# Optimization experiments

Measured on AMD Instinct MI355X. Metric: run time of the kernel, lower is better.

## Reference

```python
import jax, jax.numpy as jnp
import numpy as np

POWER = 2.0
EPS = jnp.float32(np.finfo(np.float32).eps)


def setup_inputs() -> dict:
    key = jax.random.key(0)
    k1, k2, k3 = jax.random.split(key, 3)
    B, P, S = 2, 131072, 512
    station_coords = jax.random.uniform(k1, (B, S, 2), dtype=jnp.float32)
    station_values = jax.random.normal(k2, (B, S), dtype=jnp.float32)
    grid_points = jax.random.uniform(k3, (B, P, 2), dtype=jnp.float32)
    return {
        "station_coords": station_coords,
        "station_values": station_values,
        "grid_points": grid_points,
    }


def reference(station_coords, station_values, grid_points):
    # grid_points: (B, P, 2); station_coords: (B, S, 2)
    diff = grid_points[:, :, None, :] - station_coords[:, None, :, :]  # (B, P, S, 2)
    distances = jnp.sqrt(jnp.sum(diff * diff, axis=-1))                # (B, P, S)
    distances = jnp.where(distances == 0, EPS, distances)
    weights = 1.0 / distances ** POWER                                  # (B, P, S)
    weights_sum = jnp.sum(weights, axis=-1)                             # (B, P)
    interpolated = jnp.sum(weights * station_values[:, None, :], axis=-1) / weights_sum
    return interpolated  # (B, P)
```

## Files before the change

kernel.cpp:

```cpp
#include <hip/hip_runtime.h>


#define BLOCK 256
#define GPT 8
#define NSPLIT 4
#define S_TOT 512
#define S_SUB (S_TOT / NSPLIT)

__device__ __forceinline__ void quad_op(float gx, float gy, float& ws, float& vs,
                                        const float4& f0, const float4& f1,
                                        const float4& f2) {
    constexpr float EPS  = 1.1920928955078125e-07f;
    constexpr float EPS2 = EPS * EPS;
    const float dxa = gx - f0.x, dya = gy - f0.y;
    const float a = fmaf(dxa, dxa, fmaf(dya, dya, EPS2));
    const float dxb = gx - f0.w, dyb = gy - f1.x;
    const float bq = fmaf(dxb, dxb, fmaf(dyb, dyb, EPS2));
    const float dxc = gx - f1.z, dyc = gy - f1.w;
    const float c = fmaf(dxc, dxc, fmaf(dyc, dyc, EPS2));
    const float dxd = gx - f2.y, dyd = gy - f2.z;
    const float d = fmaf(dxd, dxd, fmaf(dyd, dyd, EPS2));
    const float pab = a * bq, pcd = c * d;
    const float sab = a + bq, scd = c + d;
    const float nab = fmaf(f1.y, a, f0.z * bq);
    const float ncd = fmaf(f2.w, c, f2.x * d);
    const float r = __builtin_amdgcn_rcpf(pab * pcd);
    ws = fmaf(fmaf(sab, pcd, scd * pab), r, ws);
    vs = fmaf(fmaf(nab, pcd, ncd * pab), r, vs);
}

__global__ __launch_bounds__(BLOCK) void idw_main(
    const float* __restrict__ station_coords,
    const float* __restrict__ station_values,
    const float* __restrict__ grid_points,
    float2* __restrict__ partial,
    int P, int S) {

    __shared__ float st[S_SUB * 3];

    const int b = blockIdx.y;
    const int z = blockIdx.z;
    const float2* __restrict__ sc2 =
        (const float2*)station_coords + (size_t)b * S + z * S_SUB;
    const float* __restrict__ svb = station_values + (size_t)b * S + z * S_SUB;

    if (threadIdx.x < S_SUB) {
        const int i = threadIdx.x;
        const float2 c = sc2[i];
        st[3 * i + 0] = c.x;
        st[3 * i + 1] = c.y;
        st[3 * i + 2] = svb[i];
    }
    __syncthreads();

    const int tid = blockIdx.x * BLOCK + threadIdx.x;
    const float4* __restrict__ gp4 = (const float4*)grid_points + (size_t)b * (P / 2);
    const float4 ga = gp4[4 * tid + 0];
    const float4 gb = gp4[4 * tid + 1];
    const float4 gc = gp4[4 * tid + 2];
    const float4 gd = gp4[4 * tid + 3];
    const float gx0 = ga.x, gy0 = ga.y, gx1 = ga.z, gy1 = ga.w;
    const float gx2 = gb.x, gy2 = gb.y, gx3 = gb.z, gy3 = gb.w;
    const float gx4 = gc.x, gy4 = gc.y, gx5 = gc.z, gy5 = gc.w;
    const float gx6 = gd.x, gy6 = gd.y, gx7 = gd.z, gy7 = gd.w;

    float ws0 = 0.0f, vs0 = 0.0f, ws1 = 0.0f, vs1 = 0.0f;
    float ws2 = 0.0f, vs2 = 0.0f, ws3 = 0.0f, vs3 = 0.0f;
    float ws4 = 0.0f, vs4 = 0.0f, ws5 = 0.0f, vs5 = 0.0f;
    float ws6 = 0.0f, vs6 = 0.0f, ws7 = 0.0f, vs7 = 0.0f;

    const float4* __restrict__ st4 = (const float4*)st;

#pragma unroll 2
    for (int k = 0; k < S_SUB / 4; ++k) {
        const float4 f0 = st4[3 * k + 0];
        const float4 f1 = st4[3 * k + 1];
        const float4 f2 = st4[3 * k + 2];
        quad_op(gx0, gy0, ws0, vs0, f0, f1, f2);
        quad_op(gx1, gy1, ws1, vs1, f0, f1, f2);
        quad_op(gx2, gy2, ws2, vs2, f0, f1, f2);
        quad_op(gx3, gy3, ws3, vs3, f0, f1, f2);
        quad_op(gx4, gy4, ws4, vs4, f0, f1, f2);
        quad_op(gx5, gy5, ws5, vs5, f0, f1, f2);
        quad_op(gx6, gy6, ws6, vs6, f0, f1, f2);
        quad_op(gx7, gy7, ws7, vs7, f0, f1, f2);
    }

    float4* __restrict__ pb4 =
        (float4*)(partial + ((size_t)(z * 2 + b)) * P);
    pb4[4 * tid + 0] = make_float4(ws0, vs0, ws1, vs1);
    pb4[4 * tid + 1] = make_float4(ws2, vs2, ws3, vs3);
    pb4[4 * tid + 2] = make_float4(ws4, vs4, ws5, vs5);
    pb4[4 * tid + 3] = make_float4(ws6, vs6, ws7, vs7);
}

__global__ __launch_bounds__(256) void idw_combine(
    const float2* __restrict__ partial, float* __restrict__ out, int P) {
    const int gid = blockIdx.x * 256 + threadIdx.x;
    const int pp0 = gid * 4;
    const int b = pp0 >> 17;
    const int p0 = pp0 & (131072 - 1);

    float wa = 0.f, va = 0.f, wb = 0.f, vb = 0.f, wc = 0.f, vc = 0.f, wd = 0.f, vd = 0.f;
#pragma unroll
    for (int z = 0; z < NSPLIT; ++z) {
        const float4* __restrict__ src =
            (const float4*)(partial + ((size_t)(z * 2 + b)) * P);
        const float4 lo = src[p0 / 2 + 0];
        const float4 hi = src[p0 / 2 + 1];
        wa += lo.x; va += lo.y; wb += lo.z; vb += lo.w;
        wc += hi.x; vc += hi.y; wd += hi.z; vd += hi.w;
    }
    ((float4*)out)[((size_t)b * P + p0) / 4] =
        make_float4(va / wa, vb / wb, vc / wc, vd / wd);
}

__global__ __launch_bounds__(BLOCK) void idw_single(
    const float* __restrict__ station_coords, const float* __restrict__ station_values,
    const float* __restrict__ grid_points, float* __restrict__ out, int P, int S) {
    __shared__ float st[S_TOT * 3];
    const int b = blockIdx.y;
    const float2* __restrict__ sc2 = (const float2*)station_coords + (size_t)b * S;
    const float* __restrict__ svb = station_values + (size_t)b * S;
    for (int i = threadIdx.x; i < S; i += BLOCK) {
        const float2 c = sc2[i];
        st[3 * i + 0] = c.x; st[3 * i + 1] = c.y; st[3 * i + 2] = svb[i];
    }
    __syncthreads();
    const int tid = blockIdx.x * BLOCK + threadIdx.x;
    const float4* __restrict__ gp4 = (const float4*)grid_points + (size_t)b * (P / 2);
    const float4 ga = gp4[2 * tid + 0];
    const float4 gb = gp4[2 * tid + 1];
    float ws0 = 0, vs0 = 0, ws1 = 0, vs1 = 0, ws2 = 0, vs2 = 0, ws3 = 0, vs3 = 0;
    const float4* __restrict__ st4 = (const float4*)st;
#pragma unroll 4
    for (int k = 0; k < S_TOT / 4; ++k) {
        const float4 f0 = st4[3 * k + 0];
        const float4 f1 = st4[3 * k + 1];
        const float4 f2 = st4[3 * k + 2];
        quad_op(ga.x, ga.y, ws0, vs0, f0, f1, f2);
        quad_op(ga.z, ga.w, ws1, vs1, f0, f1, f2);
        quad_op(gb.x, gb.y, ws2, vs2, f0, f1, f2);
        quad_op(gb.z, gb.w, ws3, vs3, f0, f1, f2);
    }
    ((float4*)out)[(size_t)b * (P / 4) + tid] =
        make_float4(vs0 / ws0, vs1 / ws1, vs2 / ws2, vs3 / ws3);
}

extern "C" void kernel_launch(void* const* d_in, const int* in_sizes, int n_in,
                              void* d_out, int out_size, void* d_ws, size_t ws_size,
                              hipStream_t stream) {
    const float* station_coords = (const float*)d_in[0];
    const float* station_values = (const float*)d_in[1];
    const float* grid_points    = (const float*)d_in[2];
    float* out = (float*)d_out;

    const int B = 2;
    const int S = in_sizes[1] / B;
    const int P = out_size / B;

    const size_t need = (size_t)NSPLIT * B * P * sizeof(float2);
    if (ws_size >= need && d_ws != nullptr) {
        float2* partial = (float2*)d_ws;
        dim3 grid(P / (BLOCK * GPT), B, NSPLIT);
        idw_main<<<grid, dim3(BLOCK), 0, stream>>>(
            station_coords, station_values, grid_points, partial, P, S);
        dim3 cgrid((B * P) / (256 * 4));
        idw_combine<<<cgrid, dim3(256), 0, stream>>>(partial, out, P);
    } else {
        dim3 grid(P / (BLOCK * 4), B);
        idw_single<<<grid, dim3(BLOCK), 0, stream>>>(
            station_coords, station_values, grid_points, out, P, S);
    }
}
```

Baseline: 87.08 us.

## Read station data directly from global memory and halve station split

The main kernel drops the shared-memory staging of station coordinates and values and instead loads them as float4s straight from global memory. The loads are wave-uniform, so the compiler may turn them into scalar loads. The station split drops from four to two, which halves the partial buffer traffic and the grid size, and launch bounds now request one block per SM. The risk is fewer blocks for latency hiding and dependence on cache hits for the uniform station loads. The fallback single kernel is only restructured with a lambda.

```diff
diff --git a/kernel.cpp b/kernel.cpp
--- a/kernel.cpp
+++ b/kernel.cpp
@@ -3,55 +3,46 @@
 
 #define BLOCK 256
 #define GPT 8
-#define NSPLIT 4
+#define NSPLIT 2
 #define S_TOT 512
 #define S_SUB (S_TOT / NSPLIT)
 
-__device__ __forceinline__ void quad_op(float gx, float gy, float& ws, float& vs,
-                                        const float4& f0, const float4& f1,
-                                        const float4& f2) {
+__device__ __forceinline__ void quad_sm(float gx, float gy, float& ws, float& vs,
+                                        const float4& c0, const float4& c1,
+                                        const float4& vv) {
     constexpr float EPS  = 1.1920928955078125e-07f;
     constexpr float EPS2 = EPS * EPS;
-    const float dxa = gx - f0.x, dya = gy - f0.y;
+    const float dxa = c0.x - gx, dya = c0.y - gy;
     const float a = fmaf(dxa, dxa, fmaf(dya, dya, EPS2));
-    const float dxb = gx - f0.w, dyb = gy - f1.x;
+    const float dxb = c0.z - gx, dyb = c0.w - gy;
     const float bq = fmaf(dxb, dxb, fmaf(dyb, dyb, EPS2));
-    const float dxc = gx - f1.z, dyc = gy - f1.w;
+    const float dxc = c1.x - gx, dyc = c1.y - gy;
     const float c = fmaf(dxc, dxc, fmaf(dyc, dyc, EPS2));
-    const float dxd = gx - f2.y, dyd = gy - f2.z;
+    const float dxd = c1.z - gx, dyd = c1.w - gy;
     const float d = fmaf(dxd, dxd, fmaf(dyd, dyd, EPS2));
     const float pab = a * bq, pcd = c * d;
     const float sab = a + bq, scd = c + d;
-    const float nab = fmaf(f1.y, a, f0.z * bq);
-    const float ncd = fmaf(f2.w, c, f2.x * d);
+    const float nab = fmaf(vv.y, a, vv.x * bq);
+    const float ncd = fmaf(vv.w, c, vv.z * d);
     const float r = __builtin_amdgcn_rcpf(pab * pcd);
     ws = fmaf(fmaf(sab, pcd, scd * pab), r, ws);
     vs = fmaf(fmaf(nab, pcd, ncd * pab), r, vs);
 }
 
-__global__ __launch_bounds__(BLOCK) void idw_main(
+__global__ __launch_bounds__(BLOCK, 1) void idw_main(
     const float* __restrict__ station_coords,
     const float* __restrict__ station_values,
     const float* __restrict__ grid_points,
     float2* __restrict__ partial,
     int P, int S) {
 
-    __shared__ float st[S_SUB * 3];
-
     const int b = blockIdx.y;
     const int z = blockIdx.z;
-    const float2* __restrict__ sc2 =
-        (const float2*)station_coords + (size_t)b * S + z * S_SUB;
-    const float* __restrict__ svb = station_values + (size_t)b * S + z * S_SUB;
 
-    if (threadIdx.x < S_SUB) {
-        const int i = threadIdx.x;
-        const float2 c = sc2[i];
-        st[3 * i + 0] = c.x;
-        st[3 * i + 1] = c.y;
-        st[3 * i + 2] = svb[i];
-    }
-    __syncthreads();
+    const float4* __restrict__ sc4 =
+        (const float4*)station_coords + (size_t)b * (S_TOT / 2) + z * (S_SUB / 2);
+    const float4* __restrict__ sv4 =
+        (const float4*)station_values + (size_t)b * (S_TOT / 4) + z * (S_SUB / 4);
 
     const int tid = blockIdx.x * BLOCK + threadIdx.x;
     const float4* __restrict__ gp4 = (const float4*)grid_points + (size_t)b * (P / 2);
@@ -69,25 +60,22 @@
     float ws4 = 0.0f, vs4 = 0.0f, ws5 = 0.0f, vs5 = 0.0f;
     float ws6 = 0.0f, vs6 = 0.0f, ws7 = 0.0f, vs7 = 0.0f;
 
-    const float4* __restrict__ st4 = (const float4*)st;
-
-#pragma unroll 2
+#pragma unroll 4
     for (int k = 0; k < S_SUB / 4; ++k) {
-        const float4 f0 = st4[3 * k + 0];
-        const float4 f1 = st4[3 * k + 1];
-        const float4 f2 = st4[3 * k + 2];
-        quad_op(gx0, gy0, ws0, vs0, f0, f1, f2);
-        quad_op(gx1, gy1, ws1, vs1, f0, f1, f2);
-        quad_op(gx2, gy2, ws2, vs2, f0, f1, f2);
-        quad_op(gx3, gy3, ws3, vs3, f0, f1, f2);
-        quad_op(gx4, gy4, ws4, vs4, f0, f1, f2);
-        quad_op(gx5, gy5, ws5, vs5, f0, f1, f2);
-        quad_op(gx6, gy6, ws6, vs6, f0, f1, f2);
-        quad_op(gx7, gy7, ws7, vs7, f0, f1, f2);
+        const float4 c0 = sc4[2 * k + 0];
+        const float4 c1 = sc4[2 * k + 1];
+        const float4 vv = sv4[k];
+        quad_sm(gx0, gy0, ws0, vs0, c0, c1, vv);
+        quad_sm(gx1, gy1, ws1, vs1, c0, c1, vv);
+        quad_sm(gx2, gy2, ws2, vs2, c0, c1, vv);
+        quad_sm(gx3, gy3, ws3, vs3, c0, c1, vv);
+        quad_sm(gx4, gy4, ws4, vs4, c0, c1, vv);
+        quad_sm(gx5, gy5, ws5, vs5, c0, c1, vv);
+        quad_sm(gx6, gy6, ws6, vs6, c0, c1, vv);
+        quad_sm(gx7, gy7, ws7, vs7, c0, c1, vv);
     }
 
-    float4* __restrict__ pb4 =
-        (float4*)(partial + ((size_t)(z * 2 + b)) * P);
+    float4* __restrict__ pb4 = (float4*)(partial + ((size_t)(z * 2 + b)) * P);
     pb4[4 * tid + 0] = make_float4(ws0, vs0, ws1, vs1);
     pb4[4 * tid + 1] = make_float4(ws2, vs2, ws3, vs3);
     pb4[4 * tid + 2] = make_float4(ws4, vs4, ws5, vs5);
@@ -101,7 +89,8 @@
     const int b = pp0 >> 17;
     const int p0 = pp0 & (131072 - 1);
 
-    float wa = 0.f, va = 0.f, wb = 0.f, vb = 0.f, wc = 0.f, vc = 0.f, wd = 0.f, vd = 0.f;
+    float wa = 0.f, va = 0.f, wb = 0.f, vb = 0.f;
+    float wc = 0.f, vc = 0.f, wd = 0.f, vd = 0.f;
 #pragma unroll
     for (int z = 0; z < NSPLIT; ++z) {
         const float4* __restrict__ src =
@@ -133,15 +122,34 @@
     const float4 gb = gp4[2 * tid + 1];
     float ws0 = 0, vs0 = 0, ws1 = 0, vs1 = 0, ws2 = 0, vs2 = 0, ws3 = 0, vs3 = 0;
     const float4* __restrict__ st4 = (const float4*)st;
+    constexpr float EPS = 1.1920928955078125e-07f;
+    constexpr float EPS2 = EPS * EPS;
 #pragma unroll 4
     for (int k = 0; k < S_TOT / 4; ++k) {
         const float4 f0 = st4[3 * k + 0];
         const float4 f1 = st4[3 * k + 1];
         const float4 f2 = st4[3 * k + 2];
-        quad_op(ga.x, ga.y, ws0, vs0, f0, f1, f2);
-        quad_op(ga.z, ga.w, ws1, vs1, f0, f1, f2);
-        quad_op(gb.x, gb.y, ws2, vs2, f0, f1, f2);
-        quad_op(gb.z, gb.w, ws3, vs3, f0, f1, f2);
+        auto q = [&](float gx, float gy, float& ws, float& vs) {
+            const float dxa = gx - f0.x, dya = gy - f0.y;
+            const float a = fmaf(dxa, dxa, fmaf(dya, dya, EPS2));
+            const float dxb = gx - f0.w, dyb = gy - f1.x;
+            const float bq = fmaf(dxb, dxb, fmaf(dyb, dyb, EPS2));
+            const float dxc = gx - f1.z, dyc = gy - f1.w;
+            const float c = fmaf(dxc, dxc, fmaf(dyc, dyc, EPS2));
+            const float dxd = gx - f2.y, dyd = gy - f2.z;
+            const float d = fmaf(dxd, dxd, fmaf(dyd, dyd, EPS2));
+            const float pab = a * bq, pcd = c * d;
+            const float sab = a + bq, scd = c + d;
+            const float nab = fmaf(f1.y, a, f0.z * bq);
+            const float ncd = fmaf(f2.w, c, f2.x * d);
+            const float r = __builtin_amdgcn_rcpf(pab * pcd);
+            ws = fmaf(fmaf(sab, pcd, scd * pab), r, ws);
+            vs = fmaf(fmaf(nab, pcd, ncd * pab), r, vs);
+        };
+        q(ga.x, ga.y, ws0, vs0);
+        q(ga.z, ga.w, ws1, vs1);
+        q(gb.x, gb.y, ws2, vs2);
+        q(gb.z, gb.w, ws3, vs3);
     }
     ((float4*)out)[(size_t)b * (P / 4) + tid] =
         make_float4(vs0 / ws0, vs1 / ws1, vs2 / ws2, vs3 / ws3);
```

After: 93.52 us. +7.4%, slower.
